# Kernel tuning notes

Hardware: AMD Instinct MI355X
Metric: run time of the kernel (lower is better)

The kernel has to match this reference:

```python
import jax, jax.numpy as jnp
import numpy as np

VOCAB = 198
DEPTH = 512
NPAIR = (DEPTH - 1) // 2  # 255: columns 510,511 left as zero (matches original loop bound)


def _positional_matrix(seq_len):
    i = jnp.arange(seq_len, dtype=jnp.float32)[:, None]          # [L,1]
    j = jnp.arange(NPAIR, dtype=jnp.float32)[None, :]            # [1,255]
    angle = i / jnp.power(10000.0, 2.0 * j / DEPTH)              # [L,255]
    pe = jnp.zeros((seq_len, DEPTH), dtype=jnp.float32)
    pe = pe.at[:, 0:2 * NPAIR:2].set(jnp.sin(angle))
    pe = pe.at[:, 1:2 * NPAIR:2].set(jnp.cos(angle))
    return pe


def setup_inputs() -> dict:
    key = jax.random.key(0)
    k1, k2 = jax.random.split(key)
    idx = jax.random.randint(k1, (131072,), 0, VOCAB, dtype=jnp.int32)
    wordlist = jax.random.normal(k2, (VOCAB, DEPTH), dtype=jnp.float32)
    return {"idx": idx, "wordlist": wordlist}


def reference(idx, wordlist):
    # gather token embeddings: [L, DEPTH]
    emb = wordlist[idx]
    pe = _positional_matrix(idx.shape[0])
    return emb + pe
```

## Files before the change

kernel.cpp:

```cpp
#include <hip/hip_runtime.h>


#define L_TOTAL 131072
#define VEC_PER_ROW 128

__device__ __forceinline__ void sincos_fast(float a, float& s, float& c) {
    const float INV2PI = 0.15915493667125702f;
    const float PI2_HI = 6.2831854820251465f;
    const float PI2_LO = -1.7484555314695172e-7f;
    float k = rintf(a * INV2PI);
    float r = fmaf(-k, PI2_HI, a);
    r = fmaf(-k, PI2_LO, r);
    float rev = r * INV2PI;
    s = __builtin_amdgcn_sinf(rev);
    c = __builtin_amdgcn_cosf(rev);
}

__global__ __launch_bounds__(256) void embed_pe_kernel(
    const int* __restrict__ idx,
    const float* __restrict__ wordlist,
    float* __restrict__ out)
{
    int g = blockIdx.x * 256 + threadIdx.x;
    int i = g >> 7;
    int c = g & 127;

    int token = idx[i];
    const float4 w = ((const float4*)wordlist)[token * VEC_PER_ROW + c];

    const float K = 0.051905126483205076f;
    float j0 = (float)(2 * c);
    float j1 = (float)(2 * c + 1);
    float invf0 = exp2f(-j0 * K);
    float invf1 = exp2f(-j1 * K);
    float fi = (float)i;
    float a0 = fi * invf0;
    float a1 = fi * invf1;

    float s0, c0, s1, c1;
    sincos_fast(a0, s0, c0);
    sincos_fast(a1, s1, c1);
    if (c == VEC_PER_ROW - 1) {
        s1 = 0.0f;
        c1 = 0.0f;
    }

    float4 o;
    o.x = w.x + s0;
    o.y = w.y + c0;
    o.z = w.z + s1;
    o.w = w.w + c1;
    ((float4*)out)[g] = o;
}

extern "C" void kernel_launch(void* const* d_in, const int* in_sizes, int n_in,
                              void* d_out, int out_size, void* d_ws, size_t ws_size,
                              hipStream_t stream) {
    const int*   idx      = (const int*)d_in[0];
    const float* wordlist = (const float*)d_in[1];
    float*       out      = (float*)d_out;

    int total_vec = L_TOTAL * VEC_PER_ROW;
    int block = 256;
    int grid = total_vec / block;
    embed_pe_kernel<<<grid, block, 0, stream>>>(idx, wordlist, out);
}
```

Baseline: 285.6 us.

## Process four rows per thread using angle-addition recurrence for positional sin/cos

Each thread now handles four consecutive sequence rows for the same column vector. It computes sin/cos once at the first row, then advances to the next rows with the angle-addition rotation instead of fresh transcendental evaluations. This cuts the exp2 and sincos work per output and amortizes index math. The recurrence can accumulate rounding error over the steps, and the grid becomes four times smaller, which lowers the number of threads available to hide memory latency in a write-bound kernel.

```diff
diff --git a/kernel.cpp b/kernel.cpp
--- a/kernel.cpp
+++ b/kernel.cpp
@@ -3,6 +3,7 @@
 
 #define L_TOTAL 131072
 #define VEC_PER_ROW 128
+#define R 4
 
 __device__ __forceinline__ void sincos_fast(float a, float& s, float& c) {
     const float INV2PI = 0.15915493667125702f;
@@ -21,36 +22,46 @@
     const float* __restrict__ wordlist,
     float* __restrict__ out)
 {
-    int g = blockIdx.x * 256 + threadIdx.x;
-    int i = g >> 7;
-    int c = g & 127;
-
-    int token = idx[i];
-    const float4 w = ((const float4*)wordlist)[token * VEC_PER_ROW + c];
+    int t  = blockIdx.x * 256 + threadIdx.x;
+    int rb = t >> 7;
+    int cc = t & 127;
+    int i0 = rb * R;
 
     const float K = 0.051905126483205076f;
-    float j0 = (float)(2 * c);
-    float j1 = (float)(2 * c + 1);
-    float invf0 = exp2f(-j0 * K);
-    float invf1 = exp2f(-j1 * K);
-    float fi = (float)i;
-    float a0 = fi * invf0;
-    float a1 = fi * invf1;
+    float invf0 = exp2f(-(float)(2 * cc)     * K);
+    float invf1 = exp2f(-(float)(2 * cc + 1) * K);
 
-    float s0, c0, s1, c1;
-    sincos_fast(a0, s0, c0);
-    sincos_fast(a1, s1, c1);
-    if (c == VEC_PER_ROW - 1) {
-        s1 = 0.0f;
-        c1 = 0.0f;
+    float s0, c0, s1, c1, sd0, cd0, sd1, cd1;
+    sincos_fast((float)i0 * invf0, s0, c0);
+    sincos_fast((float)i0 * invf1, s1, c1);
+    sincos_fast(invf0, sd0, cd0);
+    sincos_fast(invf1, sd1, cd1);
+
+    bool last = (cc == VEC_PER_ROW - 1);
+
+    int tokens[R];
+#pragma unroll
+    for (int k = 0; k < R; ++k) tokens[k] = idx[i0 + k];
+
+#pragma unroll
+    for (int k = 0; k < R; ++k) {
+        float4 w = ((const float4*)wordlist)[tokens[k] * VEC_PER_ROW + cc];
+        float ps1 = last ? 0.0f : s1;
+        float pc1 = last ? 0.0f : c1;
+        float4 o;
+        o.x = w.x + s0;
+        o.y = w.y + c0;
+        o.z = w.z + ps1;
+        o.w = w.w + pc1;
+        ((float4*)out)[(i0 + k) * VEC_PER_ROW + cc] = o;
+
+        float ns0 = fmaf(s0, cd0, c0 * sd0);
+        float nc0 = fmaf(c0, cd0, -s0 * sd0);
+        s0 = ns0; c0 = nc0;
+        float ns1 = fmaf(s1, cd1, c1 * sd1);
+        float nc1 = fmaf(c1, cd1, -s1 * sd1);
+        s1 = ns1; c1 = nc1;
     }
-
-    float4 o;
-    o.x = w.x + s0;
-    o.y = w.y + c0;
-    o.z = w.z + s1;
-    o.w = w.w + c1;
-    ((float4*)out)[g] = o;
 }
 
 extern "C" void kernel_launch(void* const* d_in, const int* in_sizes, int n_in,
@@ -60,8 +71,8 @@
     const float* wordlist = (const float*)d_in[1];
     float*       out      = (float*)d_out;
 
-    int total_vec = L_TOTAL * VEC_PER_ROW;
+    int total_threads = (L_TOTAL / R) * VEC_PER_ROW;
     int block = 256;
-    int grid = total_vec / block;
+    int grid = total_threads / block;
     embed_pe_kernel<<<grid, block, 0, stream>>>(idx, wordlist, out);
 }
```

Measured after the change: 254.9 us. 10.7% less time.
